# Performance work log

Measured on AMD Instinct MI355X. Metric: run time of the kernel, lower is better.

Reference implementation:

```python
import jax, jax.numpy as jnp
import numpy as np

B, N, M, G = 2, 8192, 8192, 256
X_MIN = Y_MIN = -35.0
CELL = abs(2.0 * X_MIN / G)  # cell size, as in construct_batched_cuda_grid


def setup_inputs() -> dict:
    key = jax.random.key(0)
    k1, k2, k3, k4, k5 = jax.random.split(key, 5)
    p_i = jax.random.uniform(k1, (B, N, 3), jnp.float32, -34.0, 34.0)
    p_j = jax.random.uniform(k2, (B, M, 3), jnp.float32, -34.0, 34.0)
    mos = jax.random.normal(k3, (B, 2, G, G), jnp.float32)
    error_p_i_flow = jax.random.uniform(k4, (B, N), jnp.float32)
    nearest_flow = jax.random.randint(k5, (B, N, 1), 0, M, jnp.int32)
    return {"p_i": p_i, "mos": mos, "p_j": p_j,
            "error_p_i_flow": error_p_i_flow, "nearest_flow": nearest_flow}


def _knn1_l1(x, y):
    # brute-force 1-NN with L1 (norm=1) distance, matching knn_points(..., K=1, norm=1)
    # build (B,N,M) dist one coordinate at a time to avoid a (B,N,M,3) intermediate
    d = (jnp.abs(x[:, :, None, 0] - y[:, None, :, 0])
         + jnp.abs(x[:, :, None, 1] - y[:, None, :, 1])
         + jnp.abs(x[:, :, None, 2] - y[:, None, :, 2]))
    return jnp.min(d, axis=-1), jnp.argmin(d, axis=-1)


def reference(p_i, mos, p_j, error_p_i_flow, nearest_flow):
    # NN_loss with reduction='none' -> error_p_i_rigid = (cham_x + cham_y)/2 (needs N==M)
    cham_x, nearest_rigid = _knn1_l1(p_i, p_j)  # (B,N), (B,N)
    cham_y, _ = _knn1_l1(p_j, p_i)              # (B,M)
    error_p_i_rigid = (cham_x + cham_y) * 0.5

    dynamic = error_p_i_flow > error_p_i_rigid             # (B,N) bool
    idx = jnp.where(dynamic, nearest_flow[..., 0], nearest_rigid)  # (B,N)
    art_labels = dynamic.astype(jnp.int32)                 # (B,N) in {0,1}

    # batched gather p_j[b, idx[b]]
    p_j_by_nn = jnp.take_along_axis(p_j, idx[..., None], axis=1)  # (B,N,3)

    # construct_batched_cuda_grid: scatter labels into (B,G,G), -1 elsewhere
    shift = jnp.array([X_MIN, Y_MIN], jnp.float32)
    cell_idx = ((p_j_by_nn[:, :, :2] - shift) / CELL).astype(jnp.int32)  # (B,N,2)
    bs = jnp.repeat(jnp.arange(B), N)
    grid = -jnp.ones((B, G, G), jnp.int32)
    grid = grid.at[bs,
                   cell_idx[..., 0].reshape(-1),
                   cell_idx[..., 1].reshape(-1)].set(art_labels.reshape(-1))

    # CrossEntropyLoss(ignore_index=-1), mean over non-ignored cells
    logp = jax.nn.log_softmax(mos, axis=1)                 # (B,C,G,G)
    valid = grid >= 0
    tgt = jnp.clip(grid, 0, None)
    lp = jnp.take_along_axis(logp, tgt[:, None], axis=1)[:, 0]  # (B,G,G)
    loss = -jnp.where(valid, lp, 0.0).sum() / jnp.maximum(valid.sum(), 1).astype(lp.dtype)
    return loss
```

## Files before the change

### kernel.cpp

```cpp
#include <hip/hip_runtime.h>
#include <float.h>

#define B_ 2
#define N_ 8192
#define G_ 256
constexpr float X_MIN_F = -35.0f;
constexpr float CELL_F  = 0.2734375f;

using u64 = unsigned long long;

#define OFF_ACCUM 524288
#define OFF_PX    524352

template<int CC>
__global__ __launch_bounds__(256) void nn_kernel(const float* __restrict__ p_i,
                                                 const float* __restrict__ p_j,
                                                 u64* __restrict__ px,
                                                 float* __restrict__ colpart,
                                                 int* __restrict__ grid,
                                                 unsigned* __restrict__ accum)
{
    constexpr int COLS = N_ / CC;
    constexpr int NB   = 16 * CC;
    const int b    = blockIdx.z;
    const int tid  = threadIdx.x;
    const int lane = tid & 63;
    const int w    = tid >> 6;
    const int row0 = blockIdx.x * 1024 + tid * 4;
    const int c0   = blockIdx.y * COLS;

    __shared__ __align__(16) float q[COLS * 3];
    __shared__ float sc[4][8][35];
    __shared__ float colW[4][COLS];

    const float* __restrict__ Qg = p_j + ((size_t)b * N_ + c0) * 3;

    for (int t = tid; t < COLS * 3 / 4; t += 256)
        ((float4*)q)[t] = ((const float4*)Qg)[t];

    {
        const int lin = blockIdx.x + 8 * (blockIdx.y + CC * blockIdx.z);
        constexpr int PER = 32768 / NB;
        if (tid < PER)
            ((uint4*)grid)[lin * PER + tid] = make_uint4(~0u, ~0u, ~0u, ~0u);
        if (lin == 0 && tid < 4) accum[tid] = 0u;
    }

    const float4* pp = (const float4*)(p_i + ((size_t)b * N_ + row0) * 3);
    float4 r0 = pp[0], r1 = pp[1], r2 = pp[2];
    float px_[4] = {r0.x, r0.w, r1.z, r2.y};
    float py_[4] = {r0.y, r1.x, r1.w, r2.z};
    float pz_[4] = {r0.z, r1.y, r2.x, r2.w};

    float best[4] = {FLT_MAX, FLT_MAX, FLT_MAX, FLT_MAX};
    int   gcol[4] = {0, 0, 0, 0};

    for (int jg = 0; jg < COLS; jg += 8) {
        const float4* qv = (const float4*)(Qg + (size_t)jg * 3);
        float4 v0 = qv[0], v1 = qv[1], v2 = qv[2];
        float4 v3 = qv[3], v4 = qv[4], v5 = qv[5];
        float qx[8] = {v0.x, v0.w, v1.z, v2.y, v3.x, v3.w, v4.z, v5.y};
        float qy[8] = {v0.y, v1.x, v1.w, v2.z, v3.y, v4.x, v4.w, v5.z};
        float qz[8] = {v0.z, v1.y, v2.x, v2.w, v3.z, v4.y, v5.x, v5.w};

        float dm[4][8];
#pragma unroll
        for (int r = 0; r < 4; r++) {
#pragma unroll
            for (int k = 0; k < 8; k++)
                dm[r][k] = (fabsf(px_[r] - qx[k]) + fabsf(py_[r] - qy[k]))
                           + fabsf(pz_[r] - qz[k]);
            float m = fminf(fminf(dm[r][0], dm[r][1]), dm[r][2]);
            m = fminf(fminf(m, dm[r][3]), dm[r][4]);
            m = fminf(fminf(m, dm[r][5]), dm[r][6]);
            m = fminf(m, dm[r][7]);
            bool lt = m < best[r];
            best[r] = lt ? m : best[r];
            gcol[r] = lt ? jg : gcol[r];
        }

        float part[8];
#pragma unroll
        for (int k = 0; k < 8; k++)
            part[k] = fminf(fminf(fminf(dm[0][k], dm[1][k]), dm[2][k]),
                            dm[3][k]);

#pragma unroll
        for (int k = 0; k < 8; k++) {
            unsigned a = __float_as_uint(part[k]);
            auto pr = __builtin_amdgcn_permlane32_swap(a, a, false, false);
            part[k] = fminf(__uint_as_float(pr[0]), __uint_as_float(pr[1]));
        }
#pragma unroll
        for (int k = 0; k < 8; k++)
            sc[w][k][lane & 31] = part[k];
        const int kc = lane >> 3, mc = lane & 7;
        float c4 = fminf(fminf(sc[w][kc][4 * mc],     sc[w][kc][4 * mc + 1]),
                         fminf(sc[w][kc][4 * mc + 2], sc[w][kc][4 * mc + 3]));
        c4 = fminf(c4, __shfl_xor(c4, 1));
        c4 = fminf(c4, __shfl_xor(c4, 2));
        c4 = fminf(c4, __shfl_xor(c4, 4));
        if (mc == 0) colW[w][jg + kc] = c4;
    }

    __syncthreads();

    for (int t = tid; t < COLS; t += 256) {
        float c = fminf(fminf(colW[0][t], colW[1][t]),
                        fminf(colW[2][t], colW[3][t]));
        colpart[(size_t)blockIdx.x * (B_ * N_) + (size_t)b * N_ + c0 + t] = c;
    }

    int bidx[4];
#pragma unroll
    for (int r = 0; r < 4; r++) {
        const float4* qv = (const float4*)&q[gcol[r] * 3];
        float4 v0 = qv[0], v1 = qv[1], v2 = qv[2];
        float4 v3 = qv[3], v4 = qv[4], v5 = qv[5];
        float qx[8] = {v0.x, v0.w, v1.z, v2.y, v3.x, v3.w, v4.z, v5.y};
        float qy[8] = {v0.y, v1.x, v1.w, v2.z, v3.y, v4.x, v4.w, v5.z};
        float qz[8] = {v0.z, v1.y, v2.x, v2.w, v3.z, v4.y, v5.x, v5.w};
        int kk = 0;
#pragma unroll
        for (int k = 7; k >= 0; k--) {
            float d = (fabsf(px_[r] - qx[k]) + fabsf(py_[r] - qy[k]))
                      + fabsf(pz_[r] - qz[k]);
            kk = (d == best[r]) ? k : kk;
        }
        bidx[r] = c0 + gcol[r] + kk;
    }
    const size_t o = (size_t)blockIdx.y * (B_ * N_) + b * N_ + row0;
#pragma unroll
    for (int r = 0; r < 4; r++)
        px[o + r] = ((u64)__float_as_uint(best[r]) << 32) | (unsigned)bidx[r];
}

template<int CC>
__global__ __launch_bounds__(256) void reduce_scatter_kernel(
    const u64* __restrict__ px, const float* __restrict__ cp,
    const float* __restrict__ flow, const int* __restrict__ nflow,
    const float* __restrict__ Pj, int* __restrict__ grid)
{
    __shared__ u64      sbx[64];
    __shared__ unsigned sby[64];
    const int tid = threadIdx.x;
    const int p   = tid & 63;
    const int g   = tid >> 6;
    constexpr int CPG = CC / 4;

    if (tid < 64) { sbx[tid] = ~0ull; sby[tid] = ~0u; }
    __syncthreads();

    const int pt = blockIdx.x * 64 + p;
    u64 bx = ~0ull;
#pragma unroll
    for (int k = 0; k < CPG; k++) {
        int c = g * CPG + k;
        u64 v = px[(size_t)c * (B_ * N_) + pt];
        bx = v < bx ? v : bx;
    }
    float by = fminf(cp[(size_t)(2 * g)     * (B_ * N_) + pt],
                     cp[(size_t)(2 * g + 1) * (B_ * N_) + pt]);
    atomicMin(&sbx[p], bx);
    atomicMin(&sby[p], __float_as_uint(by));
    __syncthreads();

    if (tid < 64) {
        u64 fx = sbx[tid];
        float dx = __uint_as_float((unsigned)(fx >> 32));
        float dy = __uint_as_float(sby[tid]);
        float rigid = (dx + dy) * 0.5f;

        const int i = blockIdx.x * 64 + tid;
        const int b = i >> 13;
        const int n = i & (N_ - 1);

        bool dyn  = flow[i] > rigid;
        int label = dyn ? 1 : 0;
        int idx   = dyn ? nflow[i] : (int)(unsigned)(fx & 0xFFFFFFFFull);

        const float* qp = Pj + ((size_t)b * N_ + idx) * 3;
        float xx = qp[0], yy = qp[1];

        int cx = (int)((xx - X_MIN_F) / CELL_F);
        int cy = (int)((yy - X_MIN_F) / CELL_F);

        atomicMax(&grid[(b << 16) + cx * G_ + cy], (n << 1) | label);
    }
}

__global__ __launch_bounds__(256) void ce_kernel(const float* __restrict__ mos,
                                                 const int* __restrict__ grid,
                                                 float* __restrict__ accum,
                                                 float* __restrict__ out)
{
    int i = blockIdx.x * 256 + threadIdx.x;
    float lsum = 0.0f;
    int   lcnt = 0;

    int packed = grid[i];
    if (packed >= 0) {
        int b    = i >> 16;
        int cell = i & 0xFFFF;
        float m0 = mos[((size_t)b * 2 + 0) * 65536 + cell];
        float m1 = mos[((size_t)b * 2 + 1) * 65536 + cell];
        float mx = fmaxf(m0, m1);
        float lse = logf(expf(m0 - mx) + expf(m1 - mx));
        float sh  = ((packed & 1) ? m1 : m0) - mx;
        lsum = sh - lse;
        lcnt = 1;
    }

#pragma unroll
    for (int o = 32; o > 0; o >>= 1) {
        lsum += __shfl_down(lsum, o);
        lcnt += __shfl_down(lcnt, o);
    }
    __shared__ float wsum[4];
    __shared__ int   wcnt[4];
    int wave = threadIdx.x >> 6;
    if ((threadIdx.x & 63) == 0) { wsum[wave] = lsum; wcnt[wave] = lcnt; }
    __syncthreads();
    if (threadIdx.x == 0) {
        float s = wsum[0] + wsum[1] + wsum[2] + wsum[3];
        int   c = wcnt[0] + wcnt[1] + wcnt[2] + wcnt[3];
        atomicAdd(&accum[0], s);
        atomicAdd((int*)&accum[1], c);
        __threadfence();
        unsigned t = atomicAdd((unsigned*)&accum[2], 1u);
        if (t == gridDim.x - 1) {
            float S = atomicAdd(&accum[0], 0.0f);
            int   C = atomicAdd((int*)&accum[1], 0);
            out[0] = -S / (float)(C > 0 ? C : 1);
        }
    }
}

template<int CC>
static void run(const float* p_i, const float* mos, const float* p_j,
                const float* flow, const int* nflow, float* out,
                char* ws, hipStream_t stream)
{
    int*   grid    = (int*)ws;
    float* accum   = (float*)(ws + OFF_ACCUM);
    u64*   px      = (u64*)(ws + OFF_PX);
    float* colpart = (float*)(ws + OFF_PX + (size_t)CC * B_ * N_ * 8);

    dim3 g(8, CC, 2);
    nn_kernel<CC><<<g, 256, 0, stream>>>(p_i, p_j, px, colpart, (int*)grid,
                                         (unsigned*)accum);
    reduce_scatter_kernel<CC><<<256, 256, 0, stream>>>(px, colpart, flow,
                                                       nflow, p_j, grid);
    ce_kernel<<<(B_ * G_ * G_) / 256, 256, 0, stream>>>(mos, grid, accum, out);
}

extern "C" void kernel_launch(void* const* d_in, const int* in_sizes, int n_in,
                              void* d_out, int out_size, void* d_ws, size_t ws_size,
                              hipStream_t stream)
{
    const float* p_i   = (const float*)d_in[0];
    const float* mos   = (const float*)d_in[1];
    const float* p_j   = (const float*)d_in[2];
    const float* flow  = (const float*)d_in[3];
    const int*   nflow = (const int*)d_in[4];
    float* out = (float*)d_out;
    char* ws = (char*)d_ws;

    constexpr size_t CPART = (size_t)8 * B_ * N_ * 4;
    if (ws_size >= OFF_PX + (size_t)64 * B_ * N_ * 8 + CPART)
        run<64>(p_i, mos, p_j, flow, nflow, out, ws, stream);
    else if (ws_size >= OFF_PX + (size_t)32 * B_ * N_ * 8 + CPART)
        run<32>(p_i, mos, p_j, flow, nflow, out, ws, stream);
    else
        run<8>(p_i, mos, p_j, flow, nflow, out, ws, stream);
}
```

Baseline: 116.8 us.

## Process eight rows per thread and read query tiles from shared memory

Each thread now computes 8 rows instead of 4, so each block covers 2048 rows and the row-block count halves. The inner loop reads query points from the LDS copy instead of global memory, and the column-min scratch is padded and read as float4. The gain comes from more reuse of each query load per distance and less cross-block column-partial traffic, since the reduce kernel now reads only 4 partials. The cost is higher register pressure and half as many blocks, which may lower occupancy.

After: 117.6 us. Within noise of the previous version (+0.7%).

```diff
diff --git a/kernel.cpp b/kernel.cpp
--- a/kernel.cpp
+++ b/kernel.cpp
@@ -21,69 +21,97 @@
                                                  unsigned* __restrict__ accum)
 {
     constexpr int COLS = N_ / CC;
-    constexpr int NB   = 16 * CC;
     const int b    = blockIdx.z;
     const int tid  = threadIdx.x;
     const int lane = tid & 63;
     const int w    = tid >> 6;
-    const int row0 = blockIdx.x * 1024 + tid * 4;
+    const int row0 = blockIdx.x * 2048 + tid * 8;
     const int c0   = blockIdx.y * COLS;
 
     __shared__ __align__(16) float q[COLS * 3];
-    __shared__ float sc[4][8][35];
+    __shared__ __align__(16) float sc[4][8][36];
     __shared__ float colW[4][COLS];
 
     const float* __restrict__ Qg = p_j + ((size_t)b * N_ + c0) * 3;
-
     for (int t = tid; t < COLS * 3 / 4; t += 256)
         ((float4*)q)[t] = ((const float4*)Qg)[t];
 
     {
-        const int lin = blockIdx.x + 8 * (blockIdx.y + CC * blockIdx.z);
+        const int lin = blockIdx.x + 4 * (blockIdx.y + CC * blockIdx.z);
+        constexpr int NB  = 8 * CC;
         constexpr int PER = 32768 / NB;
-        if (tid < PER)
-            ((uint4*)grid)[lin * PER + tid] = make_uint4(~0u, ~0u, ~0u, ~0u);
+        for (int t = tid; t < PER; t += 256)
+            ((uint4*)grid)[lin * PER + t] = make_uint4(~0u, ~0u, ~0u, ~0u);
         if (lin == 0 && tid < 4) accum[tid] = 0u;
     }
 
     const float4* pp = (const float4*)(p_i + ((size_t)b * N_ + row0) * 3);
-    float4 r0 = pp[0], r1 = pp[1], r2 = pp[2];
-    float px_[4] = {r0.x, r0.w, r1.z, r2.y};
-    float py_[4] = {r0.y, r1.x, r1.w, r2.z};
-    float pz_[4] = {r0.z, r1.y, r2.x, r2.w};
-
-    float best[4] = {FLT_MAX, FLT_MAX, FLT_MAX, FLT_MAX};
-    int   gcol[4] = {0, 0, 0, 0};
+    float4 a0 = pp[0], a1 = pp[1], a2 = pp[2];
+    float4 a3 = pp[3], a4 = pp[4], a5 = pp[5];
+    float px_[8] = {a0.x, a0.w, a1.z, a2.y, a3.x, a3.w, a4.z, a5.y};
+    float py_[8] = {a0.y, a1.x, a1.w, a2.z, a3.y, a4.x, a4.w, a5.z};
+    float pz_[8] = {a0.z, a1.y, a2.x, a2.w, a3.z, a4.y, a5.x, a5.w};
+
+    float best[8];
+    int   gcol[8];
+#pragma unroll
+    for (int r = 0; r < 8; r++) { best[r] = FLT_MAX; gcol[r] = 0; }
+
+    __syncthreads();
 
     for (int jg = 0; jg < COLS; jg += 8) {
-        const float4* qv = (const float4*)(Qg + (size_t)jg * 3);
+        const float4* qv = (const float4*)&q[jg * 3];
         float4 v0 = qv[0], v1 = qv[1], v2 = qv[2];
         float4 v3 = qv[3], v4 = qv[4], v5 = qv[5];
         float qx[8] = {v0.x, v0.w, v1.z, v2.y, v3.x, v3.w, v4.z, v5.y};
         float qy[8] = {v0.y, v1.x, v1.w, v2.z, v3.y, v4.x, v4.w, v5.z};
         float qz[8] = {v0.z, v1.y, v2.x, v2.w, v3.z, v4.y, v5.x, v5.w};
 
-        float dm[4][8];
-#pragma unroll
-        for (int r = 0; r < 4; r++) {
+        float part[8];
+        {
+            float dm[4][8];
+#pragma unroll
+            for (int r = 0; r < 4; r++) {
+#pragma unroll
+                for (int k = 0; k < 8; k++)
+                    dm[r][k] = (fabsf(px_[r] - qx[k]) + fabsf(py_[r] - qy[k]))
+                               + fabsf(pz_[r] - qz[k]);
+                float m = fminf(fminf(dm[r][0], dm[r][1]), dm[r][2]);
+                m = fminf(fminf(m, dm[r][3]), dm[r][4]);
+                m = fminf(fminf(m, dm[r][5]), dm[r][6]);
+                m = fminf(m, dm[r][7]);
+                bool lt = m < best[r];
+                best[r] = lt ? m : best[r];
+                gcol[r] = lt ? jg : gcol[r];
+            }
 #pragma unroll
             for (int k = 0; k < 8; k++)
-                dm[r][k] = (fabsf(px_[r] - qx[k]) + fabsf(py_[r] - qy[k]))
-                           + fabsf(pz_[r] - qz[k]);
-            float m = fminf(fminf(dm[r][0], dm[r][1]), dm[r][2]);
-            m = fminf(fminf(m, dm[r][3]), dm[r][4]);
-            m = fminf(fminf(m, dm[r][5]), dm[r][6]);
-            m = fminf(m, dm[r][7]);
-            bool lt = m < best[r];
-            best[r] = lt ? m : best[r];
-            gcol[r] = lt ? jg : gcol[r];
-        }
-
-        float part[8];
-#pragma unroll
-        for (int k = 0; k < 8; k++)
-            part[k] = fminf(fminf(fminf(dm[0][k], dm[1][k]), dm[2][k]),
-                            dm[3][k]);
+                part[k] = fminf(fminf(fminf(dm[0][k], dm[1][k]), dm[2][k]),
+                                dm[3][k]);
+        }
+        {
+            float dm[4][8];
+#pragma unroll
+            for (int r = 0; r < 4; r++) {
+                const int rr = r + 4;
+#pragma unroll
+                for (int k = 0; k < 8; k++)
+                    dm[r][k] = (fabsf(px_[rr] - qx[k]) + fabsf(py_[rr] - qy[k]))
+                               + fabsf(pz_[rr] - qz[k]);
+                float m = fminf(fminf(dm[r][0], dm[r][1]), dm[r][2]);
+                m = fminf(fminf(m, dm[r][3]), dm[r][4]);
+                m = fminf(fminf(m, dm[r][5]), dm[r][6]);
+                m = fminf(m, dm[r][7]);
+                bool lt = m < best[rr];
+                best[rr] = lt ? m : best[rr];
+                gcol[rr] = lt ? jg : gcol[rr];
+            }
+#pragma unroll
+            for (int k = 0; k < 8; k++)
+                part[k] = fminf(part[k],
+                                fminf(fminf(fminf(dm[0][k], dm[1][k]),
+                                            dm[2][k]), dm[3][k]));
+        }
 
 #pragma unroll
         for (int k = 0; k < 8; k++) {
@@ -95,8 +123,8 @@
         for (int k = 0; k < 8; k++)
             sc[w][k][lane & 31] = part[k];
         const int kc = lane >> 3, mc = lane & 7;
-        float c4 = fminf(fminf(sc[w][kc][4 * mc],     sc[w][kc][4 * mc + 1]),
-                         fminf(sc[w][kc][4 * mc + 2], sc[w][kc][4 * mc + 3]));
+        float4 c4v = *(const float4*)&sc[w][kc][4 * mc];
+        float c4 = fminf(fminf(c4v.x, c4v.y), fminf(c4v.z, c4v.w));
         c4 = fminf(c4, __shfl_xor(c4, 1));
         c4 = fminf(c4, __shfl_xor(c4, 2));
         c4 = fminf(c4, __shfl_xor(c4, 4));
@@ -111,9 +139,9 @@
         colpart[(size_t)blockIdx.x * (B_ * N_) + (size_t)b * N_ + c0 + t] = c;
     }
 
-    int bidx[4];
-#pragma unroll
-    for (int r = 0; r < 4; r++) {
+    int bidx[8];
+#pragma unroll
+    for (int r = 0; r < 8; r++) {
         const float4* qv = (const float4*)&q[gcol[r] * 3];
         float4 v0 = qv[0], v1 = qv[1], v2 = qv[2];
         float4 v3 = qv[3], v4 = qv[4], v5 = qv[5];
@@ -131,7 +159,7 @@
     }
     const size_t o = (size_t)blockIdx.y * (B_ * N_) + b * N_ + row0;
 #pragma unroll
-    for (int r = 0; r < 4; r++)
+    for (int r = 0; r < 8; r++)
         px[o + r] = ((u64)__float_as_uint(best[r]) << 32) | (unsigned)bidx[r];
 }
 
@@ -159,8 +187,7 @@
         u64 v = px[(size_t)c * (B_ * N_) + pt];
         bx = v < bx ? v : bx;
     }
-    float by = fminf(cp[(size_t)(2 * g)     * (B_ * N_) + pt],
-                     cp[(size_t)(2 * g + 1) * (B_ * N_) + pt]);
+    float by = cp[(size_t)g * (B_ * N_) + pt];
     atomicMin(&sbx[p], bx);
     atomicMin(&sby[p], __float_as_uint(by));
     __syncthreads();
@@ -246,7 +273,7 @@
     u64*   px      = (u64*)(ws + OFF_PX);
     float* colpart = (float*)(ws + OFF_PX + (size_t)CC * B_ * N_ * 8);
 
-    dim3 g(8, CC, 2);
+    dim3 g(4, CC, 2);
     nn_kernel<CC><<<g, 256, 0, stream>>>(p_i, p_j, px, colpart, (int*)grid,
                                          (unsigned*)accum);
     reduce_scatter_kernel<CC><<<256, 256, 0, stream>>>(px, colpart, flow,
@@ -266,11 +293,11 @@
     float* out = (float*)d_out;
     char* ws = (char*)d_ws;
 
-    constexpr size_t CPART = (size_t)8 * B_ * N_ * 4;
+    constexpr size_t CPART = (size_t)4 * B_ * N_ * 4;
     if (ws_size >= OFF_PX + (size_t)64 * B_ * N_ * 8 + CPART)
         run<64>(p_i, mos, p_j, flow, nflow, out, ws, stream);
-    else if (ws_size >= OFF_PX + (size_t)32 * B_ * N_ * 8 + CPART)
-        run<32>(p_i, mos, p_j, flow, nflow, out, ws, stream);
+    else if (ws_size >= OFF_PX + (size_t)16 * B_ * N_ * 8 + CPART)
+        run<16>(p_i, mos, p_j, flow, nflow, out, ws, stream);
     else
         run<8>(p_i, mos, p_j, flow, nflow, out, ws, stream);
 }
```

## Fuse cross-entropy into reduce-scatter kernel via grid-wide spin barrier

Applied to the files above, without the earlier changes.

Merges the cross-entropy reduction into the reduce/scatter kernel, which drops one kernel launch. After scattering, all 256 blocks wait on a global atomic counter acting as a grid barrier. Each point then checks whether its packed value won the atomicMax for its cell and, if so, adds that cell's log-softmax term. This visits only occupied cells instead of scanning all 131072 grid cells, at the cost of relying on all 256 blocks being co-resident for the spin barrier. The mid-tier fallback also changes from CC=32 to CC=16.

After: 121.1 us. 3.7% more time.

```diff
diff --git a/kernel.cpp b/kernel.cpp
--- a/kernel.cpp
+++ b/kernel.cpp
@@ -21,7 +21,6 @@
                                                  unsigned* __restrict__ accum)
 {
     constexpr int COLS = N_ / CC;
-    constexpr int NB   = 16 * CC;
     const int b    = blockIdx.z;
     const int tid  = threadIdx.x;
     const int lane = tid & 63;
@@ -34,12 +33,12 @@
     __shared__ float colW[4][COLS];
 
     const float* __restrict__ Qg = p_j + ((size_t)b * N_ + c0) * 3;
-
     for (int t = tid; t < COLS * 3 / 4; t += 256)
         ((float4*)q)[t] = ((const float4*)Qg)[t];
 
     {
         const int lin = blockIdx.x + 8 * (blockIdx.y + CC * blockIdx.z);
+        constexpr int NB  = 16 * CC;
         constexpr int PER = 32768 / NB;
         if (tid < PER)
             ((uint4*)grid)[lin * PER + tid] = make_uint4(~0u, ~0u, ~0u, ~0u);
@@ -136,10 +135,12 @@
 }
 
 template<int CC>
-__global__ __launch_bounds__(256) void reduce_scatter_kernel(
+__global__ __launch_bounds__(256) void reduce_scatter_ce_kernel(
     const u64* __restrict__ px, const float* __restrict__ cp,
     const float* __restrict__ flow, const int* __restrict__ nflow,
-    const float* __restrict__ Pj, int* __restrict__ grid)
+    const float* __restrict__ Pj, const float* __restrict__ mos,
+    int* __restrict__ grid, unsigned* __restrict__ accum,
+    float* __restrict__ out)
 {
     __shared__ u64      sbx[64];
     __shared__ unsigned sby[64];
@@ -165,6 +166,7 @@
     atomicMin(&sby[p], __float_as_uint(by));
     __syncthreads();
 
+    int gidx = 0, packed_mine = -2, bb = 0, cell = 0;
     if (tid < 64) {
         u64 fx = sbx[tid];
         float dx = __uint_as_float((unsigned)(fx >> 32));
@@ -172,66 +174,63 @@
         float rigid = (dx + dy) * 0.5f;
 
         const int i = blockIdx.x * 64 + tid;
-        const int b = i >> 13;
+        bb = i >> 13;
         const int n = i & (N_ - 1);
 
         bool dyn  = flow[i] > rigid;
         int label = dyn ? 1 : 0;
         int idx   = dyn ? nflow[i] : (int)(unsigned)(fx & 0xFFFFFFFFull);
 
-        const float* qp = Pj + ((size_t)b * N_ + idx) * 3;
+        const float* qp = Pj + ((size_t)bb * N_ + idx) * 3;
         float xx = qp[0], yy = qp[1];
 
         int cx = (int)((xx - X_MIN_F) / CELL_F);
         int cy = (int)((yy - X_MIN_F) / CELL_F);
 
-        atomicMax(&grid[(b << 16) + cx * G_ + cy], (n << 1) | label);
-    }
-}
-
-__global__ __launch_bounds__(256) void ce_kernel(const float* __restrict__ mos,
-                                                 const int* __restrict__ grid,
-                                                 float* __restrict__ accum,
-                                                 float* __restrict__ out)
-{
-    int i = blockIdx.x * 256 + threadIdx.x;
-    float lsum = 0.0f;
-    int   lcnt = 0;
-
-    int packed = grid[i];
-    if (packed >= 0) {
-        int b    = i >> 16;
-        int cell = i & 0xFFFF;
-        float m0 = mos[((size_t)b * 2 + 0) * 65536 + cell];
-        float m1 = mos[((size_t)b * 2 + 1) * 65536 + cell];
-        float mx = fmaxf(m0, m1);
-        float lse = logf(expf(m0 - mx) + expf(m1 - mx));
-        float sh  = ((packed & 1) ? m1 : m0) - mx;
-        lsum = sh - lse;
-        lcnt = 1;
-    }
-
-#pragma unroll
-    for (int o = 32; o > 0; o >>= 1) {
-        lsum += __shfl_down(lsum, o);
-        lcnt += __shfl_down(lcnt, o);
-    }
-    __shared__ float wsum[4];
-    __shared__ int   wcnt[4];
-    int wave = threadIdx.x >> 6;
-    if ((threadIdx.x & 63) == 0) { wsum[wave] = lsum; wcnt[wave] = lcnt; }
-    __syncthreads();
-    if (threadIdx.x == 0) {
-        float s = wsum[0] + wsum[1] + wsum[2] + wsum[3];
-        int   c = wcnt[0] + wcnt[1] + wcnt[2] + wcnt[3];
-        atomicAdd(&accum[0], s);
-        atomicAdd((int*)&accum[1], c);
+        cell = cx * G_ + cy;
+        gidx = (bb << 16) + cell;
+        packed_mine = (n << 1) | label;
+        atomicMax(&grid[gidx], packed_mine);
+    }
+
+    __syncthreads();
+    if (tid == 0) {
         __threadfence();
-        unsigned t = atomicAdd((unsigned*)&accum[2], 1u);
-        if (t == gridDim.x - 1) {
-            float S = atomicAdd(&accum[0], 0.0f);
-            int   C = atomicAdd((int*)&accum[1], 0);
-            out[0] = -S / (float)(C > 0 ? C : 1);
+        atomicAdd(&accum[2], 1u);
+        while (atomicAdd(&accum[2], 0u) < 256u)
+            __builtin_amdgcn_s_sleep(8);
+    }
+    __syncthreads();
+
+    if (tid < 64) {
+        float lsum = 0.0f;
+        int   lcnt = 0;
+        int cur = __hip_atomic_load(&grid[gidx], __ATOMIC_RELAXED,
+                                    __HIP_MEMORY_SCOPE_AGENT);
+        if (cur == packed_mine) {
+            float m0 = mos[((size_t)bb * 2 + 0) * 65536 + cell];
+            float m1 = mos[((size_t)bb * 2 + 1) * 65536 + cell];
+            float mx = fmaxf(m0, m1);
+            float lse = logf(expf(m0 - mx) + expf(m1 - mx));
+            float sh  = ((packed_mine & 1) ? m1 : m0) - mx;
+            lsum = sh - lse;
+            lcnt = 1;
+        }
+#pragma unroll
+        for (int o = 32; o > 0; o >>= 1) {
+            lsum += __shfl_down(lsum, o);
+            lcnt += __shfl_down(lcnt, o);
+        }
+        if (tid == 0) {
+            atomicAdd((float*)&accum[0], lsum);
+            atomicAdd((int*)&accum[1], lcnt);
+            __threadfence();
+            unsigned t = atomicAdd(&accum[3], 1u);
+            if (t == 255u) {
+                float S = atomicAdd((float*)&accum[0], 0.0f);
+                int   C = atomicAdd((int*)&accum[1], 0);
+                out[0] = -S / (float)(C > 0 ? C : 1);
+            }
         }
     }
 }
@@ -241,17 +240,15 @@
                 const float* flow, const int* nflow, float* out,
                 char* ws, hipStream_t stream)
 {
-    int*   grid    = (int*)ws;
-    float* accum   = (float*)(ws + OFF_ACCUM);
-    u64*   px      = (u64*)(ws + OFF_PX);
-    float* colpart = (float*)(ws + OFF_PX + (size_t)CC * B_ * N_ * 8);
+    int*      grid    = (int*)ws;
+    unsigned* accum   = (unsigned*)(ws + OFF_ACCUM);
+    u64*      px      = (u64*)(ws + OFF_PX);
+    float*    colpart = (float*)(ws + OFF_PX + (size_t)CC * B_ * N_ * 8);
 
     dim3 g(8, CC, 2);
-    nn_kernel<CC><<<g, 256, 0, stream>>>(p_i, p_j, px, colpart, (int*)grid,
-                                         (unsigned*)accum);
-    reduce_scatter_kernel<CC><<<256, 256, 0, stream>>>(px, colpart, flow,
-                                                       nflow, p_j, grid);
-    ce_kernel<<<(B_ * G_ * G_) / 256, 256, 0, stream>>>(mos, grid, accum, out);
+    nn_kernel<CC><<<g, 256, 0, stream>>>(p_i, p_j, px, colpart, grid, accum);
+    reduce_scatter_ce_kernel<CC><<<256, 256, 0, stream>>>(
+        px, colpart, flow, nflow, p_j, mos, grid, accum, out);
 }
 
 extern "C" void kernel_launch(void* const* d_in, const int* in_sizes, int n_in,
@@ -269,8 +266,8 @@
     constexpr size_t CPART = (size_t)8 * B_ * N_ * 4;
     if (ws_size >= OFF_PX + (size_t)64 * B_ * N_ * 8 + CPART)
         run<64>(p_i, mos, p_j, flow, nflow, out, ws, stream);
-    else if (ws_size >= OFF_PX + (size_t)32 * B_ * N_ * 8 + CPART)
-        run<32>(p_i, mos, p_j, flow, nflow, out, ws, stream);
+    else if (ws_size >= OFF_PX + (size_t)16 * B_ * N_ * 8 + CPART)
+        run<16>(p_i, mos, p_j, flow, nflow, out, ws, stream);
     else
         run<8>(p_i, mos, p_j, flow, nflow, out, ws, stream);
 }
```
